# Kernel optimization log

Measured on AMD Instinct MI355X. Metric: run time of the kernel, lower is better.

The kernel has to match this reference:

```python
import jax, jax.numpy as jnp
import numpy as np

B, F, H, E = 16384, 128, 64, 16


def setup_inputs() -> dict:
    key = jax.random.key(0)
    k_x, k_w1, k_b1, k_w2, k_b2 = jax.random.split(key, 5)
    # Per-feature stacked params: Linear(1,H) -> W1 [F,H], b1 [F,H];
    # Linear(H,E) -> W2 [F,E,H], b2 [F,E]. Scaled like torch default init.
    x = jax.random.normal(k_x, (B, F), dtype=jnp.float32)
    W1 = jax.random.uniform(k_w1, (F, H), jnp.float32, -1.0, 1.0)  # bound = 1/sqrt(in=1)
    b1 = jax.random.uniform(k_b1, (F, H), jnp.float32, -1.0, 1.0)
    bnd = 1.0 / np.sqrt(H)
    W2 = jax.random.uniform(k_w2, (F, E, H), jnp.float32, -bnd, bnd)
    b2 = jax.random.uniform(k_b2, (F, E), jnp.float32, -bnd, bnd)
    return {"x": x, "W1": W1, "b1": b1, "W2": W2, "b2": b2}


def reference(x, W1, b1, W2, b2) -> jnp.ndarray:
    # h[b,f,h] = relu(x[b,f] * W1[f,h] + b1[f,h])   (Linear(1,H) is a scalar-vector product)
    h = jax.nn.relu(x[:, :, None] * W1[None, :, :] + b1[None, :, :])  # [B,F,H]
    # emb[b,f,e] = sum_h h[b,f,h] * W2[f,e,h] + b2[f,e]
    emb = jnp.einsum("bfh,feh->bfe", h, W2) + b2[None, :, :]  # [B,F,E]
    # concat per-feature embeddings along last dim -> [B, F*E]
    return emb.reshape(x.shape[0], -1)
```

## Files before the change

### kernel.cpp

```cpp
#include <hip/hip_runtime.h>


#define F_   128
#define H_   64
#define E_   16
#define NROW 65
#define GRS  32
#define RS   36
#define TPF  (NROW * RS)
#define FPB  4
#define BPB  512
#define THREADS 256

__global__ __launch_bounds__(64) void build_tables(
    const float* __restrict__ W1, const float* __restrict__ B1,
    const float* __restrict__ W2, const float* __restrict__ B2,
    float* __restrict__ tbl, float* __restrict__ bps)
{
    const int f = blockIdx.x;
    const int h = threadIdx.x;

    __shared__ float ts_raw[H_];
    __shared__ float ts_sorted[H_];
    __shared__ float scS[H_];
    __shared__ float scT[H_];

    const float w1 = W1[f * H_ + h];
    const float bb = B1[f * H_ + h];
    const bool  slope = (w1 != 0.0f);
    const float t   = slope ? (-bb / w1) : __builtin_inff();
    const float sgn = slope ? (w1 > 0.0f ? 1.0f : -1.0f) : 0.0f;
    const bool act0 = (w1 < 0.0f) || (!slope && bb > 0.0f);

    ts_raw[h] = t;
    __syncthreads();
    int rank = 0;
    #pragma unroll
    for (int j = 0; j < H_; ++j) {
        float tj = ts_raw[j];
        rank += (tj < t || (tj == t && j < h)) ? 1 : 0;
    }
    ts_sorted[rank] = t;
    __syncthreads();
    bps[f * H_ + h] = ts_sorted[h];

    for (int e = 0; e < E_; ++e) {
        const float w2 = W2[(f * E_ + e) * H_ + h];
        const float dS = sgn * w1 * w2;
        const float dT = sgn * bb * w2;
        float bS = act0 ? w1 * w2 : 0.0f;
        float bT = act0 ? bb * w2 : 0.0f;
        #pragma unroll
        for (int d = 32; d; d >>= 1) { bS += __shfl_xor(bS, d); bT += __shfl_xor(bT, d); }

        __syncthreads();
        scS[rank] = dS; scT[rank] = dT;
        __syncthreads();
        float vS = scS[h], vT = scT[h];
        #pragma unroll
        for (int d = 1; d < 64; d <<= 1) {
            float uS = __shfl_up(vS, (unsigned)d);
            float uT = __shfl_up(vT, (unsigned)d);
            if (h >= d) { vS += uS; vT += uT; }
        }
        const float b2v = B2[f * E_ + e];
        float* row = tbl + ((size_t)f * NROW + (h + 1)) * GRS;
        row[e]      = bS + vS;
        row[E_ + e] = bT + vT + b2v;
        if (h == 0) {
            float* r0 = tbl + (size_t)f * NROW * GRS;
            r0[e]      = bS;
            r0[E_ + e] = bT + b2v;
        }
    }
}

__global__ __launch_bounds__(THREADS) void embed_main(
    const float* __restrict__ x, const float* __restrict__ tbl,
    const float* __restrict__ bps, float* __restrict__ out)
{
    __shared__ float lt[FPB * TPF];
    __shared__ float lb[FPB * H_];

    const int tid = threadIdx.x;
    const int f0  = blockIdx.y * FPB;

    for (int i = tid; i < FPB * NROW * 8; i += THREADS) {
        int fl = i / (NROW * 8); int r = i - fl * (NROW * 8);
        int k = r >> 3; int c4 = (r & 7) << 2;
        float4 v = *(const float4*)(tbl + ((size_t)(f0 + fl) * NROW + k) * GRS + c4);
        *(float4*)(lt + fl * TPF + k * RS + c4) = v;
    }
    for (int i = tid; i < FPB * H_ / 4; i += THREADS) {
        int fl = i >> 4; int c4 = (i & 15) << 2;
        *(float4*)(lb + fl * H_ + c4) = *(const float4*)(bps + (size_t)(f0 + fl) * H_ + c4);
    }
    __syncthreads();

    const int   fl   = tid & (FPB - 1);
    const int   bloc = tid >> 2;
    const int   f    = f0 + fl;
    const float* myb = lb + fl * H_;
    const float* myt = lt + fl * TPF;
    const int bbase  = blockIdx.x * BPB;

    float xs[BPB / 64];
    #pragma unroll
    for (int it = 0; it < BPB / 64; ++it)
        xs[it] = x[(size_t)(bbase + it * 64 + bloc) * F_ + f];

    #pragma unroll
    for (int it = 0; it < BPB / 64; ++it) {
        const int   b  = bbase + it * 64 + bloc;
        const float xv = xs[it];
        int k = 0;
        #pragma unroll
        for (int s = 64; s >= 1; s >>= 1) {
            int nk  = k + s;
            int idx = (nk <= 64) ? (nk - 1) : 63;
            bool ok = (nk <= 64) && (myb[idx] <= xv);
            if (ok) k = nk;
        }
        const float* row = myt + k * RS;
        float4 s0 = *(const float4*)(row + 0);
        float4 s1 = *(const float4*)(row + 4);
        float4 s2 = *(const float4*)(row + 8);
        float4 s3 = *(const float4*)(row + 12);
        float4 t0 = *(const float4*)(row + 16);
        float4 t1 = *(const float4*)(row + 20);
        float4 t2 = *(const float4*)(row + 24);
        float4 t3 = *(const float4*)(row + 28);
        float4 o0, o1, o2, o3;
        o0.x = fmaf(s0.x, xv, t0.x); o0.y = fmaf(s0.y, xv, t0.y);
        o0.z = fmaf(s0.z, xv, t0.z); o0.w = fmaf(s0.w, xv, t0.w);
        o1.x = fmaf(s1.x, xv, t1.x); o1.y = fmaf(s1.y, xv, t1.y);
        o1.z = fmaf(s1.z, xv, t1.z); o1.w = fmaf(s1.w, xv, t1.w);
        o2.x = fmaf(s2.x, xv, t2.x); o2.y = fmaf(s2.y, xv, t2.y);
        o2.z = fmaf(s2.z, xv, t2.z); o2.w = fmaf(s2.w, xv, t2.w);
        o3.x = fmaf(s3.x, xv, t3.x); o3.y = fmaf(s3.y, xv, t3.y);
        o3.z = fmaf(s3.z, xv, t3.z); o3.w = fmaf(s3.w, xv, t3.w);
        float4* op = (float4*)(out + (size_t)b * (F_ * E_) + f * E_);
        op[0] = o0; op[1] = o1; op[2] = o2; op[3] = o3;
    }
}

extern "C" void kernel_launch(void* const* d_in, const int* in_sizes, int n_in,
                              void* d_out, int out_size, void* d_ws, size_t ws_size,
                              hipStream_t stream) {
    const float* x  = (const float*)d_in[0];
    const float* W1 = (const float*)d_in[1];
    const float* b1 = (const float*)d_in[2];
    const float* W2 = (const float*)d_in[3];
    const float* b2 = (const float*)d_in[4];
    float* out = (float*)d_out;
    const int B = in_sizes[0] / F_;

    float* tbl = (float*)d_ws;
    float* bps = tbl + (size_t)F_ * NROW * GRS;

    build_tables<<<F_, 64, 0, stream>>>(W1, b1, W2, b2, tbl, bps);
    dim3 grid(B / BPB, F_ / FPB);
    embed_main<<<grid, THREADS, 0, stream>>>(x, tbl, bps, out);
}
```

Measured before the change: 189.1 us.

## Split embedding outputs across four lanes per row and use nontemporal stores

Each thread now writes one float4 quarter of a feature's 16-wide embedding instead of all four. Four consecutive lanes cover one feature, so 16 lanes write a contiguous 256-byte span and the stores coalesce better. Rows per block drop from 512 to 128, which quadruples the number of blocks. The binary search is now repeated in each of the four lanes, and each block reloads the shared tables, so redundant work goes up. Output stores use the nontemporal builtin to avoid polluting the cache.

```diff
diff --git a/kernel.cpp b/kernel.cpp
--- a/kernel.cpp
+++ b/kernel.cpp
@@ -9,8 +9,12 @@
 #define RS   36
 #define TPF  (NROW * RS)
 #define FPB  4
-#define BPB  512
+#define RPI  16
+#define ITERS 8
+#define BPB  (RPI * ITERS)
 #define THREADS 256
+
+typedef float vf4 __attribute__((ext_vector_type(4)));
 
 __global__ __launch_bounds__(64) void build_tables(
     const float* __restrict__ W1, const float* __restrict__ B1,
@@ -97,21 +101,22 @@
     }
     __syncthreads();
 
-    const int   fl   = tid & (FPB - 1);
-    const int   bloc = tid >> 2;
+    const int   eq   = tid & 3;
+    const int   fl   = (tid >> 2) & 3;
+    const int   rloc = tid >> 4;
     const int   f    = f0 + fl;
     const float* myb = lb + fl * H_;
     const float* myt = lt + fl * TPF;
     const int bbase  = blockIdx.x * BPB;
 
-    float xs[BPB / 64];
+    float xs[ITERS];
     #pragma unroll
-    for (int it = 0; it < BPB / 64; ++it)
-        xs[it] = x[(size_t)(bbase + it * 64 + bloc) * F_ + f];
+    for (int it = 0; it < ITERS; ++it)
+        xs[it] = x[(size_t)(bbase + it * RPI + rloc) * F_ + f];
 
     #pragma unroll
-    for (int it = 0; it < BPB / 64; ++it) {
-        const int   b  = bbase + it * 64 + bloc;
+    for (int it = 0; it < ITERS; ++it) {
+        const int   b  = bbase + it * RPI + rloc;
         const float xv = xs[it];
         int k = 0;
         #pragma unroll
@@ -121,26 +126,16 @@
             bool ok = (nk <= 64) && (myb[idx] <= xv);
             if (ok) k = nk;
         }
-        const float* row = myt + k * RS;
-        float4 s0 = *(const float4*)(row + 0);
-        float4 s1 = *(const float4*)(row + 4);
-        float4 s2 = *(const float4*)(row + 8);
-        float4 s3 = *(const float4*)(row + 12);
-        float4 t0 = *(const float4*)(row + 16);
-        float4 t1 = *(const float4*)(row + 20);
-        float4 t2 = *(const float4*)(row + 24);
-        float4 t3 = *(const float4*)(row + 28);
-        float4 o0, o1, o2, o3;
-        o0.x = fmaf(s0.x, xv, t0.x); o0.y = fmaf(s0.y, xv, t0.y);
-        o0.z = fmaf(s0.z, xv, t0.z); o0.w = fmaf(s0.w, xv, t0.w);
-        o1.x = fmaf(s1.x, xv, t1.x); o1.y = fmaf(s1.y, xv, t1.y);
-        o1.z = fmaf(s1.z, xv, t1.z); o1.w = fmaf(s1.w, xv, t1.w);
-        o2.x = fmaf(s2.x, xv, t2.x); o2.y = fmaf(s2.y, xv, t2.y);
-        o2.z = fmaf(s2.z, xv, t2.z); o2.w = fmaf(s2.w, xv, t2.w);
-        o3.x = fmaf(s3.x, xv, t3.x); o3.y = fmaf(s3.y, xv, t3.y);
-        o3.z = fmaf(s3.z, xv, t3.z); o3.w = fmaf(s3.w, xv, t3.w);
-        float4* op = (float4*)(out + (size_t)b * (F_ * E_) + f * E_);
-        op[0] = o0; op[1] = o1; op[2] = o2; op[3] = o3;
+        const float* row = myt + k * RS + eq * 4;
+        float4 S = *(const float4*)(row);
+        float4 T = *(const float4*)(row + E_);
+        vf4 o;
+        o.x = fmaf(S.x, xv, T.x);
+        o.y = fmaf(S.y, xv, T.y);
+        o.z = fmaf(S.z, xv, T.z);
+        o.w = fmaf(S.w, xv, T.w);
+        vf4* op = (vf4*)(out + (size_t)b * (F_ * E_) + f * E_ + eq * 4);
+        __builtin_nontemporal_store(o, op);
     }
 }
 
```

Result: faster. 182.8 us (-3.4%).
